# Kernel tuning notes

Hardware: AMD Instinct MI355X
Metric: run time of the kernel (lower is better)

Reference implementation:

```python
import jax, jax.numpy as jnp
import numpy as np

VOCABSIZE = 100000
EMBEDSIZE = 128
BATCH = 262144


def setup_inputs() -> dict:
    key = jax.random.key(0)
    k1, k2, k3, k4, k5 = jax.random.split(key, 5)
    xs = jax.random.randint(k1, (BATCH,), 0, VOCABSIZE, dtype=jnp.int64 if jax.config.jax_enable_x64 else jnp.int32)
    ys = jax.random.randint(k2, (BATCH,), 0, VOCABSIZE, dtype=jnp.int64 if jax.config.jax_enable_x64 else jnp.int32)
    metric = jax.random.normal(k3, (EMBEDSIZE, EMBEDSIZE), dtype=jnp.float32)
    EMBEDM = jax.random.normal(k4, (VOCABSIZE, EMBEDSIZE), dtype=jnp.float32)
    # Original inits NEGEMBEDM to zeros; we use small random values so the
    # output / gradients are non-degenerate for kernel correctness testing.
    NEGEMBEDM = jax.random.normal(k5, (VOCABSIZE, EMBEDSIZE), dtype=jnp.float32) * 0.1
    return {"xs": xs, "ys": ys, "metric": metric, "EMBEDM": EMBEDM, "NEGEMBEDM": NEGEMBEDM}


def reference(xs, ys, metric, EMBEDM, NEGEMBEDM):
    # Faithful math: diag((E[xs] @ metric) @ N[ys].T) == sum((E[xs] @ metric) * N[ys], -1).
    # We compute the batched bilinear form directly, avoiding the O(B^2*D)
    # full matmul + diag extraction of the original.
    xsembeds = EMBEDM[xs]          # [B, D]
    ysembeds = NEGEMBEDM[ys]       # [B, D]
    d = jnp.einsum('bd,de,be->b', xsembeds, metric, ysembeds)  # [B]
    return jax.nn.sigmoid(2.0 * d - 1.0)
```

## Files before the change

### kernel.cpp

```cpp
#include <hip/hip_runtime.h>
#include <hip/hip_fp16.h>

#define D        128
#define NROWS    100000
#define NET      (NROWS / 16)
#define GRID_P   768
#define NWAVES   (GRID_P * 4)

typedef __attribute__((ext_vector_type(8))) _Float16 f16x8;
typedef __attribute__((ext_vector_type(4))) _Float16 f16x4;
typedef __attribute__((ext_vector_type(4))) float    f32x4;

union F16x8U { _Float16 h[8]; f16x8 v; };
union F16x4U { _Float16 h[4]; f16x4 v; };
union F32x4U { float f[4]; f32x4 v; };

typedef __attribute__((address_space(1))) const void gvoid;
typedef __attribute__((address_space(3))) void       lvoid;

__global__ __launch_bounds__(256) void convert_M16(
    const float* __restrict__ M, _Float16* __restrict__ mh)
{
    const int q    = blockIdx.x * 256 + threadIdx.x;
    const int kk   = q >> 9;
    const int cf   = (q >> 6) & 7;
    const int lane = q & 63;
    const int col  = cf * 16 + (lane & 15);
    const int k0   = kk * 32 + (lane >> 4) * 8;

    F16x8U h;
    #pragma unroll
    for (int j = 0; j < 8; ++j) h.h[j] = (_Float16)M[(k0 + j) * D + col];
    *(f16x8*)(mh + q * 8) = h.v;
}

__global__ __launch_bounds__(256, 3) void gemm_E_pers(
    const float* __restrict__ E, const _Float16* __restrict__ mh,
    _Float16* __restrict__ Ep)
{
    __shared__ _Float16 smM[2048 * 8];
    __shared__ _Float16 scr[4][2048];

    const int tid  = threadIdx.x;
    const int lane = tid & 63;
    const int w    = tid >> 6;
    const int lrow = lane & 15;
    const int lk   = lane >> 4;

    #pragma unroll
    for (int it = 0; it < 8; ++it) {
        const int slot = it * 256 + w * 64 + lane;
        __builtin_amdgcn_global_load_lds(
            (gvoid*)(mh + slot * 8), (lvoid*)(smM + (it * 256 + w * 64) * 8),
            16, 0, 0);
    }
    asm volatile("s_waitcnt vmcnt(0)" ::: "memory");
    __syncthreads();

    const f16x8* Bh = (const f16x8*)smM;
    _Float16*    S  = scr[w];

    const int gw = (int)blockIdx.x * 4 + w;

    #pragma unroll 1
    for (int t = gw; t < NET; t += NWAVES) {
        #pragma unroll
        for (int i = 0; i < 8; ++i) {
            const int f   = i * 256 + lane * 4;
            const int row = f >> 7;
            const int col = f & 127;
            F32x4U v; v.v = *(const f32x4*)(E + (size_t)t * 2048 + f);
            F16x4U h4;
            h4.h[0] = (_Float16)v.f[0]; h4.h[1] = (_Float16)v.f[1];
            h4.h[2] = (_Float16)v.f[2]; h4.h[3] = (_Float16)v.f[3];
            const int tsl = (col >> 3) ^ row;
            *(f16x4*)(S + row * 128 + tsl * 8 + (col & 7)) = h4.v;
        }
        asm volatile("s_waitcnt lgkmcnt(0)" ::: "memory");
        __builtin_amdgcn_sched_barrier(0);

        f32x4 acc[8];
        #pragma unroll
        for (int cf = 0; cf < 8; ++cf) acc[cf] = (f32x4){0.f, 0.f, 0.f, 0.f};

        #pragma unroll
        for (int kk = 0; kk < 4; ++kk) {
            const f16x8 a16 =
                *(const f16x8*)(S + lrow * 128 + ((kk * 4 + lk) ^ lrow) * 8);
            #pragma unroll
            for (int cf = 0; cf < 8; ++cf)
                acc[cf] = __builtin_amdgcn_mfma_f32_16x16x32_f16(
                    a16, Bh[(kk * 8 + cf) * 64 + lane], acc[cf], 0, 0, 0);
        }

        #pragma unroll
        for (int i = 0; i < 4; ++i) {
            const int ro = t * 16 + lk * 4 + i;
            F16x8U o;
            #pragma unroll
            for (int cf = 0; cf < 8; ++cf) o.h[cf] = (_Float16)acc[cf][i];
            *(f16x8*)(Ep + (size_t)ro * D + lrow * 8) = o.v;
        }
    }
}

__global__ __launch_bounds__(256) void gather_dotN(
    const int* __restrict__ xs, const int* __restrict__ ys,
    const _Float16* __restrict__ Ep, const float* __restrict__ N,
    float* __restrict__ out)
{
    const int tid = threadIdx.x;
    const int o0  = blockIdx.x * 32 + (tid >> 4) * 2;
    const int l   = tid & 15;

    const int x0 = xs[o0], x1 = xs[o0 + 1];
    const int y0 = ys[o0], y1 = ys[o0 + 1];

    const f16x8 a0 = *(const f16x8*)(Ep + (size_t)x0 * D + l * 8);
    const f16x8 a1 = *(const f16x8*)(Ep + (size_t)x1 * D + l * 8);
    const float* n0 = N + (size_t)y0 * D + l;
    const float* n1 = N + (size_t)y1 * D + l;

    float r0 = 0.f, r1 = 0.f;
    #pragma unroll
    for (int j = 0; j < 8; ++j) {
        r0 += (float)a0[j] * n0[16 * j];
        r1 += (float)a1[j] * n1[16 * j];
    }

    r0 += __shfl_xor(r0, 1); r1 += __shfl_xor(r1, 1);
    r0 += __shfl_xor(r0, 2); r1 += __shfl_xor(r1, 2);
    r0 += __shfl_xor(r0, 4); r1 += __shfl_xor(r1, 4);
    r0 += __shfl_xor(r0, 8); r1 += __shfl_xor(r1, 8);

    if (l == 0) {
        float2 v;
        v.x = 1.0f / (1.0f + __expf(1.0f - 2.0f * r0));
        v.y = 1.0f / (1.0f + __expf(1.0f - 2.0f * r1));
        *(float2*)(out + o0) = v;
    }
}

extern "C" void kernel_launch(void* const* d_in, const int* in_sizes, int n_in,
                              void* d_out, int out_size, void* d_ws, size_t ws_size,
                              hipStream_t stream) {
    const int*   xs     = (const int*)d_in[0];
    const int*   ys     = (const int*)d_in[1];
    const float* metric = (const float*)d_in[2];
    const float* EMBEDM = (const float*)d_in[3];
    const float* NEGEM  = (const float*)d_in[4];
    float*       out    = (float*)d_out;

    const int B = in_sizes[0];

    char* ws = (char*)d_ws;
    _Float16* Ep = (_Float16*)ws;
    _Float16* mh = (_Float16*)(ws + (64u << 20));

    convert_M16<<<8, 256, 0, stream>>>(metric, mh);

    gemm_E_pers<<<GRID_P, 256, 0, stream>>>(EMBEDM, mh, Ep);

    gather_dotN<<<B / 32, 256, 0, stream>>>(xs, ys, Ep, NEGEM, out);
}
```

Measured before the change: 51.28 us.

## Permute metric columns so gather reads contiguous N rows, four outputs per group

The metric's column order in the f16 conversion is permuted so each lane's eight Ep values line up with eight contiguous columns of N. The gather can then load N with two 16-byte vector loads per row instead of eight strided scalar loads. Each 16-lane group now handles four outputs, with vectorised index loads and a float4 store, and the grid is halved. This aims to cut memory instructions and raise memory-level parallelism in the gather, at the cost of more registers per thread.

```diff
diff --git a/kernel.cpp b/kernel.cpp
--- a/kernel.cpp
+++ b/kernel.cpp
@@ -25,7 +25,7 @@
     const int kk   = q >> 9;
     const int cf   = (q >> 6) & 7;
     const int lane = q & 63;
-    const int col  = cf * 16 + (lane & 15);
+    const int col  = (lane & 15) * 8 + cf;
     const int k0   = kk * 32 + (lane >> 4) * 8;
 
     F16x8U h;
@@ -104,40 +104,58 @@
     }
 }
 
-__global__ __launch_bounds__(256) void gather_dotN(
+__global__ __launch_bounds__(256, 4) void gather_nat4(
     const int* __restrict__ xs, const int* __restrict__ ys,
     const _Float16* __restrict__ Ep, const float* __restrict__ N,
     float* __restrict__ out)
 {
     const int tid = threadIdx.x;
-    const int o0  = blockIdx.x * 32 + (tid >> 4) * 2;
+    const int o0  = blockIdx.x * 64 + (tid >> 4) * 4;
     const int l   = tid & 15;
 
-    const int x0 = xs[o0], x1 = xs[o0 + 1];
-    const int y0 = ys[o0], y1 = ys[o0 + 1];
+    const int4 x4 = *(const int4*)(xs + o0);
+    const int4 y4 = *(const int4*)(ys + o0);
+    const int xv[4] = {x4.x, x4.y, x4.z, x4.w};
+    const int yv[4] = {y4.x, y4.y, y4.z, y4.w};
 
-    const f16x8 a0 = *(const f16x8*)(Ep + (size_t)x0 * D + l * 8);
-    const f16x8 a1 = *(const f16x8*)(Ep + (size_t)x1 * D + l * 8);
-    const float* n0 = N + (size_t)y0 * D + l;
-    const float* n1 = N + (size_t)y1 * D + l;
-
-    float r0 = 0.f, r1 = 0.f;
+    f16x8  a[4];
+    F32x4U na[4], nb[4];
     #pragma unroll
-    for (int j = 0; j < 8; ++j) {
-        r0 += (float)a0[j] * n0[16 * j];
-        r1 += (float)a1[j] * n1[16 * j];
+    for (int q = 0; q < 4; ++q)
+        a[q] = *(const f16x8*)(Ep + (size_t)xv[q] * D + l * 8);
+    #pragma unroll
+    for (int q = 0; q < 4; ++q) {
+        na[q].v = *(const f32x4*)(N + (size_t)yv[q] * D + l * 8);
+        nb[q].v = *(const f32x4*)(N + (size_t)yv[q] * D + l * 8 + 4);
     }
 
-    r0 += __shfl_xor(r0, 1); r1 += __shfl_xor(r1, 1);
-    r0 += __shfl_xor(r0, 2); r1 += __shfl_xor(r1, 2);
-    r0 += __shfl_xor(r0, 4); r1 += __shfl_xor(r1, 4);
-    r0 += __shfl_xor(r0, 8); r1 += __shfl_xor(r1, 8);
+    float r[4];
+    #pragma unroll
+    for (int q = 0; q < 4; ++q) {
+        float s = 0.f;
+        #pragma unroll
+        for (int j = 0; j < 4; ++j) {
+            s += (float)a[q][j]     * na[q].f[j];
+            s += (float)a[q][j + 4] * nb[q].f[j];
+        }
+        r[q] = s;
+    }
+
+    #pragma unroll
+    for (int q = 0; q < 4; ++q) {
+        r[q] += __shfl_xor(r[q], 1);
+        r[q] += __shfl_xor(r[q], 2);
+        r[q] += __shfl_xor(r[q], 4);
+        r[q] += __shfl_xor(r[q], 8);
+    }
 
     if (l == 0) {
-        float2 v;
-        v.x = 1.0f / (1.0f + __expf(1.0f - 2.0f * r0));
-        v.y = 1.0f / (1.0f + __expf(1.0f - 2.0f * r1));
-        *(float2*)(out + o0) = v;
+        float4 v;
+        v.x = 1.0f / (1.0f + __expf(1.0f - 2.0f * r[0]));
+        v.y = 1.0f / (1.0f + __expf(1.0f - 2.0f * r[1]));
+        v.z = 1.0f / (1.0f + __expf(1.0f - 2.0f * r[2]));
+        v.w = 1.0f / (1.0f + __expf(1.0f - 2.0f * r[3]));
+        *(float4*)(out + o0) = v;
     }
 }
 
@@ -161,5 +179,5 @@
 
     gemm_E_pers<<<GRID_P, 256, 0, stream>>>(EMBEDM, mh, Ep);
 
-    gather_dotN<<<B / 32, 256, 0, stream>>>(xs, ys, Ep, NEGEM, out);
+    gather_nat4<<<B / 64, 256, 0, stream>>>(xs, ys, Ep, NEGEM, out);
 }
```

Result: no change. 51.46 us (+0.4%).
